# Kernel optimization log

Hardware: AMD Instinct MI355X
Metric: run time of the kernel (lower is better)

Reference implementation:

```python
import jax, jax.numpy as jnp
import numpy as np
import math

B, LQ, LK = 8, 1024, 1024
D_MODEL, NHEAD = 512, 8
DH = D_MODEL // NHEAD
FACTOR = 5
U = FACTOR * int(np.ceil(np.log(LQ)))  # 35: Informer's sample_k == n_top here (L_Q == L_K)


def _ln(x, g, b, eps=1e-5):
    m = x.mean(-1, keepdims=True)
    v = ((x - m) ** 2).mean(-1, keepdims=True)
    return (x - m) / jnp.sqrt(v + eps) * g + b


def _heads(x):  # (B,L,D) -> (B,H,L,Dh)
    Bx, L, _ = x.shape
    return x.reshape(Bx, L, NHEAD, DH).transpose(0, 2, 1, 3)


def _merge(x):  # (B,H,L,Dh) -> (B,L,D)
    Bx, H, L, Dh = x.shape
    return x.transpose(0, 2, 1, 3).reshape(Bx, L, H * Dh)


def _prob_attn(q, k, v, index_sample):
    # Informer ProbAttention, mask_flag=False. q,k,v: (B,H,L,Dh)
    Bx, H, Lq, Dh = q.shape
    Lk = k.shape[2]
    k_samp = k[:, :, index_sample, :]                        # (B,H,Lq,U,Dh) gathered keys
    qk_samp = jnp.einsum('bhld,bhlud->bhlu', q, k_samp)      # sampled scores
    M = qk_samp.max(-1) - qk_samp.sum(-1) / Lk               # sparsity measurement (B,H,Lq)
    _, top = jax.lax.top_k(M, U)                             # (B,H,U) top-u query indices
    q_red = jnp.take_along_axis(q, top[..., None], axis=2)   # (B,H,U,Dh)
    scores = jnp.einsum('bhud,bhkd->bhuk', q_red, k) * (1.0 / math.sqrt(Dh))
    attn = jax.nn.softmax(scores, axis=-1)
    upd = jnp.einsum('bhuk,bhkd->bhud', attn, v)             # (B,H,U,Dh)
    # initial context = mean of V (non-causal branch), then scatter top-u rows
    ctx = jnp.broadcast_to(v.mean(2, keepdims=True), (Bx, H, Lq, Dh))
    bi = jnp.arange(Bx)[:, None, None]
    hi = jnp.arange(H)[None, :, None]
    ctx = ctx.at[bi, hi, top].set(upd)
    return ctx


def _full_attn(q, k, v):
    s = jnp.einsum('bhld,bhsd->bhls', q, k) * (1.0 / math.sqrt(q.shape[-1]))
    a = jax.nn.softmax(s, axis=-1)
    return jnp.einsum('bhls,bhsd->bhld', a, v)


def setup_inputs():
    key = jax.random.key(0)
    ks = jax.random.split(key, 40)
    d = {}
    d['tgt'] = jax.random.normal(ks[0], (B, LQ, D_MODEL), jnp.float32)
    d['memory'] = jax.random.normal(ks[1], (B, LK, D_MODEL), jnp.float32)
    d['index_sample'] = jax.random.randint(ks[2], (LQ, U), 0, LK)
    i = 3
    for pre in ('1', '2'):
        for n in ('q', 'k', 'v', 'o'):
            d['w%s%s' % (n, pre)] = jax.random.normal(ks[i], (D_MODEL, D_MODEL), jnp.float32) * 0.02
            d['b%s%s' % (n, pre)] = jnp.zeros((D_MODEL,), jnp.float32)
            i += 1
    d['conv1_w'] = jax.random.normal(ks[i], (D_MODEL, 4 * D_MODEL), jnp.float32) * 0.02; i += 1
    d['conv1_b'] = jnp.zeros((4 * D_MODEL,), jnp.float32)
    d['conv2_w'] = jax.random.normal(ks[i], (4 * D_MODEL, D_MODEL), jnp.float32) * 0.02; i += 1
    d['conv2_b'] = jnp.zeros((D_MODEL,), jnp.float32)
    for n in ('ln1', 'ln2', 'ln3'):
        d[n + '_g'] = jnp.ones((D_MODEL,), jnp.float32)
        d[n + '_b'] = jnp.zeros((D_MODEL,), jnp.float32)
    return d


def reference(tgt, memory, index_sample, wq1, bq1, wk1, bk1, wv1, bv1, wo1, bo1,
              wq2, bq2, wk2, bk2, wv2, bv2, wo2, bo2,
              conv1_w, conv1_b, conv2_w, conv2_b,
              ln1_g, ln1_b, ln2_g, ln2_b, ln3_g, ln3_b):
    # dropout layers are identity (eval mode)
    x = tgt
    q = _heads(x @ wq1 + bq1)
    k = _heads(x @ wk1 + bk1)
    v = _heads(x @ wv1 + bv1)
    xn = _merge(_prob_attn(q, k, v, index_sample)) @ wo1 + bo1   # ProbSparse self-attn
    x = _ln(x + xn, ln1_g, ln1_b)                                # norm_enc1, with residual
    q = _heads(x @ wq2 + bq2)
    k = _heads(memory @ wk2 + bk2)
    v = _heads(memory @ wv2 + bv2)
    x = _merge(_full_attn(q, k, v)) @ wo2 + bo2                  # full cross-attn (no residual, per source)
    y = x = _ln(x, ln2_g, ln2_b)                                 # norm_enc2
    y = jax.nn.relu(y @ conv1_w + conv1_b) @ conv2_w + conv2_b   # conv1x1 FFN
    return _ln(x + y, ln3_g, ln3_b)                              # norm_enc3
```

## Files before the change

kernel.cpp:

```cpp
#include <hip/hip_runtime.h>
#include <hip/hip_bf16.h>
#include <cstdint>

constexpr int Bb  = 8;
constexpr int Ls  = 1024;
constexpr int DM  = 512;
constexpr int NH  = 8;
constexpr int DHd = 64;
constexpr int MR  = Bb * Ls;
constexpr int ZH  = Bb * NH;

typedef __attribute__((ext_vector_type(8))) short short8v;
typedef __attribute__((ext_vector_type(4))) short short4v;
typedef __attribute__((ext_vector_type(4))) float floatx4;

__device__ inline short f2bf(float x) {
  __hip_bfloat16 h = __float2bfloat16(x);
  return *reinterpret_cast<short*>(&h);
}
__device__ inline float bf2f(short s) {
  return __uint_as_float(((uint32_t)(uint16_t)s) << 16);
}

#define GLOAD_LDS16(g, l)                                                        \
  __builtin_amdgcn_global_load_lds(                                              \
      (const __attribute__((address_space(1))) void*)(g),                        \
      (__attribute__((address_space(3))) void*)(l), 16, 0, 0)

template<int MODE, int RELU>
__global__ __launch_bounds__(256) void k_gemm_mfma(
    const __hip_bfloat16* __restrict__ A, const __hip_bfloat16* __restrict__ Wt,
    const float* __restrict__ bias, const float* __restrict__ bias1,
    const float* __restrict__ bias2,
    void* __restrict__ Cout, void* __restrict__ aux1, void* __restrict__ aux2,
    void* __restrict__ aux3,
    int M, int N, int K)
{
  __shared__ __hip_bfloat16 As[2][128 * 32];
  __shared__ __hip_bfloat16 Bs[2][128 * 32];
  const int tid = threadIdx.x;
  const int w = tid >> 6, lane = tid & 63;
  const int wr = w >> 1, wc = w & 1;
  const int bm = blockIdx.x * 128, bn = blockIdx.y * 128;
  const int lrow = lane >> 2;
  const int lcol = (lane & 3) * 8;
  const int fr = lane & 15;
  const int fco = (lane >> 4) * 8;

  const __hip_bfloat16* Asrc = A;
  if (MODE == 12 && bn >= 512) Asrc = (const __hip_bfloat16*)aux3;

  const int ksl = K / gridDim.z;
  const int kb0 = blockIdx.z * ksl;
  const int nst = ksl / 32;

  const int chunk0 = w * 2, chunk1 = w * 2 + 1;
  const size_t aoff0 = (size_t)(bm + chunk0 * 16 + lrow) * K + lcol;
  const size_t aoff1 = (size_t)(bm + chunk1 * 16 + lrow) * K + lcol;
  const size_t boff0 = (size_t)(bn + chunk0 * 16 + lrow) * K + lcol;
  const size_t boff1 = (size_t)(bn + chunk1 * 16 + lrow) * K + lcol;

  {
    const int k0 = kb0;
    GLOAD_LDS16(Asrc + aoff0 + k0, &As[0][chunk0 * 512]);
    GLOAD_LDS16(Asrc + aoff1 + k0, &As[0][chunk1 * 512]);
    GLOAD_LDS16(Wt + boff0 + k0, &Bs[0][chunk0 * 512]);
    GLOAD_LDS16(Wt + boff1 + k0, &Bs[0][chunk1 * 512]);
  }
  asm volatile("s_waitcnt vmcnt(0)" ::: "memory");
  __builtin_amdgcn_s_barrier();

  floatx4 acc[4][4] = {};
  int cur = 0;
  for (int t = 0; t < nst; ++t) {
    if (t + 1 < nst) {
      const int k0 = kb0 + (t + 1) * 32;
      GLOAD_LDS16(Asrc + aoff0 + k0, &As[cur ^ 1][chunk0 * 512]);
      GLOAD_LDS16(Asrc + aoff1 + k0, &As[cur ^ 1][chunk1 * 512]);
      GLOAD_LDS16(Wt + boff0 + k0, &Bs[cur ^ 1][chunk0 * 512]);
      GLOAD_LDS16(Wt + boff1 + k0, &Bs[cur ^ 1][chunk1 * 512]);
    }
    const short* Ash = (const short*)As[cur];
    const short* Bsh = (const short*)Bs[cur];
    short8v a[4], b[4];
#pragma unroll
    for (int mi = 0; mi < 4; ++mi)
      a[mi] = *(const short8v*)(Ash + (wr * 64 + mi * 16 + fr) * 32 + fco);
#pragma unroll
    for (int ni = 0; ni < 4; ++ni)
      b[ni] = *(const short8v*)(Bsh + (wc * 64 + ni * 16 + fr) * 32 + fco);
#pragma unroll
    for (int mi = 0; mi < 4; ++mi)
#pragma unroll
      for (int ni = 0; ni < 4; ++ni)
        acc[mi][ni] = __builtin_amdgcn_mfma_f32_16x16x32_bf16(
            a[mi], b[ni], acc[mi][ni], 0, 0, 0);
    asm volatile("s_waitcnt vmcnt(0)" ::: "memory");
    __builtin_amdgcn_s_barrier();
    cur ^= 1;
  }
#pragma unroll
  for (int ni = 0; ni < 4; ++ni) {
    const int cn = bn + wc * 64 + ni * 16 + fr;
    float bv = 0.f;
    if (MODE == 10 || MODE == 12) {
      const float* bp = (cn < 512) ? bias : (cn < 1024 ? bias1 : bias2);
      bv = bp[cn & 511];
    } else if (MODE != 20) {
      bv = bias[cn];
    }
#pragma unroll
    for (int mi = 0; mi < 4; ++mi) {
      const int rm0 = bm + wr * 64 + mi * 16 + (lane >> 4) * 4;
      float vv[4];
#pragma unroll
      for (int j = 0; j < 4; ++j) {
        float v = acc[mi][ni][j] + bv;
        if (RELU) v = fmaxf(v, 0.f);
        vv[j] = v;
      }
      if (MODE == 1) {
#pragma unroll
        for (int j = 0; j < 4; ++j)
          ((__hip_bfloat16*)Cout)[(size_t)(rm0 + j) * N + cn] = __float2bfloat16(vv[j]);
      } else if (MODE == 10) {
        const int sel = cn >> 9, c = cn & 511;
        if (sel == 2) {
#pragma unroll
          for (int j = 0; j < 4; ++j)
            ((float*)aux2)[(size_t)(rm0 + j) * 512 + c] = vv[j];
        } else {
          const int hh = c >> 6, dd = c & 63;
          const int bb = rm0 >> 10, l0 = rm0 & 1023;
          __hip_bfloat16* bb16 = (__hip_bfloat16*)aux3 +
                                 (sel ? (size_t)ZH * Ls * 64 : 0);
#pragma unroll
          for (int j = 0; j < 4; ++j)
            bb16[(((size_t)(bb * 8 + hh)) * 1024 + l0 + j) * 64 + dd] =
                __float2bfloat16(vv[j]);
        }
      } else if (MODE == 12) {
        const int sel = cn >> 9, c = cn & 511;
        if (sel == 0) {
#pragma unroll
          for (int j = 0; j < 4; ++j)
            ((__hip_bfloat16*)Cout)[(size_t)(rm0 + j) * 512 + c] =
                __float2bfloat16(vv[j] * 0.125f);
        } else if (sel == 1) {
          const int cs = (c & ~63) | ((c & 63) ^ ((rm0 & 7) << 3));
#pragma unroll
          for (int j = 0; j < 4; ++j) {
            const int rm = rm0 + j;
            const int cj = (c & ~63) | ((c & 63) ^ ((rm & 7) << 3));
            ((__hip_bfloat16*)aux1)[(size_t)rm * 512 + cj] = __float2bfloat16(vv[j]);
          }
          (void)cs;
        } else {
          const int hh = c >> 6, dd = c & 63;
          const int bb = rm0 >> 10, l0 = rm0 & 1023;
          short4v pk;
#pragma unroll
          for (int j = 0; j < 4; ++j) pk[j] = f2bf(vv[j]);
          *(short4v*)((__hip_bfloat16*)aux2 +
                      (size_t)((bb * 8 + hh) * 64 + dd) * 1024 +
                      ((l0 ^ ((dd & 7) << 3)))) = pk;
        }
      } else if (MODE == 20) {
        float* pz = (float*)(blockIdx.z == 0 ? Cout :
                    blockIdx.z == 1 ? aux1 :
                    blockIdx.z == 2 ? aux2 : aux3);
#pragma unroll
        for (int j = 0; j < 4; ++j)
          pz[(size_t)(rm0 + j) * N + cn] = vv[j];
      }
    }
  }
}

__global__ __launch_bounds__(512) void k_flash2(
    const __hip_bfloat16* __restrict__ Qb,
    const __hip_bfloat16* __restrict__ Kb,
    const __hip_bfloat16* __restrict__ Vt,
    __hip_bfloat16* __restrict__ O)
{
  __shared__ __hip_bfloat16 Ks[2][64 * 64];
  __shared__ __hip_bfloat16 Vs[2][64 * 64];
  __shared__ __hip_bfloat16 Ps[8 * 16 * 72];
  const int tid = threadIdx.x, w = tid >> 6, lane = tid & 63;
  const int g = lane >> 4, r = lane & 15;
  const int z = blockIdx.y, b = z >> 3, h = z & 7;
  const int q0 = blockIdx.x * 128 + w * 16;
  __hip_bfloat16* Pw = Ps + w * 16 * 72;

  const int srow = w * 8 + (lane >> 3);
  const int sseg = lane & 7;

  const short8v qf0 = *(const short8v*)(Qb + (size_t)(b * Ls + q0 + r) * DM + h * DHd + g * 8);
  const short8v qf1 = *(const short8v*)(Qb + (size_t)(b * Ls + q0 + r) * DM + h * DHd + 32 + g * 8);

  floatx4 oacc[4] = {};
  float m_run = -1e30f, l_run = 0.f;

  GLOAD_LDS16(Kb + (size_t)(b * Ls + srow) * DM + h * DHd + sseg * 8, &Ks[0][w * 512]);
  GLOAD_LDS16(Vt + ((size_t)z * DHd + srow) * Ls + sseg * 8, &Vs[0][w * 512]);
  asm volatile("s_waitcnt vmcnt(0)" ::: "memory");
  __builtin_amdgcn_s_barrier();

  int cur = 0;
  for (int t = 0; t < 16; ++t) {
    if (t + 1 < 16) {
      GLOAD_LDS16(Kb + (size_t)(b * Ls + (t + 1) * 64 + srow) * DM + h * DHd + sseg * 8,
                  &Ks[cur ^ 1][w * 512]);
      GLOAD_LDS16(Vt + ((size_t)z * DHd + srow) * Ls + (t + 1) * 64 + sseg * 8,
                  &Vs[cur ^ 1][w * 512]);
    }
    const __hip_bfloat16* Kc = Ks[cur];
    const __hip_bfloat16* Vc = Vs[cur];
    float sv[4][4];
    float tmax = -1e30f;
    __builtin_amdgcn_s_setprio(1);
#pragma unroll
    for (int kt = 0; kt < 4; ++kt) {
      const int key = kt * 16 + r, sw = key & 7;
      short8v a0 = *(const short8v*)(Kc + key * 64 + ((g ^ sw) * 8));
      short8v a1 = *(const short8v*)(Kc + key * 64 + (((4 + g) ^ sw) * 8));
      floatx4 c = {};
      c = __builtin_amdgcn_mfma_f32_16x16x32_bf16(a0, qf0, c, 0, 0, 0);
      c = __builtin_amdgcn_mfma_f32_16x16x32_bf16(a1, qf1, c, 0, 0, 0);
#pragma unroll
      for (int j = 0; j < 4; ++j) {
        float x = c[j];
        sv[kt][j] = x;
        tmax = fmaxf(tmax, x);
      }
    }
    __builtin_amdgcn_s_setprio(0);
    tmax = fmaxf(tmax, __shfl_xor(tmax, 16));
    tmax = fmaxf(tmax, __shfl_xor(tmax, 32));
    float m_new;
    if (__all(tmax <= m_run + 8.0f)) {
      m_new = m_run;
    } else {
      m_new = fmaxf(m_run, tmax);
      const float fac = __expf(m_run - m_new);
      float fj[4];
#pragma unroll
      for (int j = 0; j < 4; ++j) fj[j] = __shfl(fac, (lane & 48) | (g * 4 + j));
#pragma unroll
      for (int ct = 0; ct < 4; ++ct)
#pragma unroll
        for (int j = 0; j < 4; ++j) oacc[ct][j] *= fj[j];
      l_run *= fac;
    }
    float psum = 0.f;
#pragma unroll
    for (int kt = 0; kt < 4; ++kt) {
      short4v pk;
#pragma unroll
      for (int j = 0; j < 4; ++j) {
        float p = __expf(sv[kt][j] - m_new);
        psum += p;
        pk[j] = f2bf(p);
      }
      *(short4v*)(Pw + r * 72 + kt * 16 + g * 4) = pk;
    }
    psum += __shfl_xor(psum, 16);
    psum += __shfl_xor(psum, 32);
    l_run += psum;
    m_run = m_new;
    const short8v pa0 = *(const short8v*)(Pw + r * 72 + g * 8);
    const short8v pa1 = *(const short8v*)(Pw + r * 72 + 32 + g * 8);
    __builtin_amdgcn_s_setprio(1);
#pragma unroll
    for (int ct = 0; ct < 4; ++ct) {
      const int d = ct * 16 + r, sw = d & 7;
      short8v v0 = *(const short8v*)(Vc + d * 64 + ((g ^ sw) * 8));
      short8v v1 = *(const short8v*)(Vc + d * 64 + (((4 + g) ^ sw) * 8));
      oacc[ct] = __builtin_amdgcn_mfma_f32_16x16x32_bf16(pa0, v0, oacc[ct], 0, 0, 0);
      oacc[ct] = __builtin_amdgcn_mfma_f32_16x16x32_bf16(pa1, v1, oacc[ct], 0, 0, 0);
    }
    __builtin_amdgcn_s_setprio(0);
    asm volatile("s_waitcnt vmcnt(0)" ::: "memory");
    __builtin_amdgcn_s_barrier();
    cur ^= 1;
  }
  float li[4];
#pragma unroll
  for (int j = 0; j < 4; ++j)
    li[j] = 1.0f / __shfl(l_run, (lane & 48) | (g * 4 + j));
#pragma unroll
  for (int ct = 0; ct < 4; ++ct)
#pragma unroll
    for (int j = 0; j < 4; ++j)
      O[(size_t)(b * Ls + q0 + g * 4 + j) * DM + h * DHd + ct * 16 + r] =
          __float2bfloat16(oacc[ct][j] * li[j]);
}

struct CvtArgs { const float* s[12]; __hip_bfloat16* d[12]; };
__global__ __launch_bounds__(256) void k_cvt_all(CvtArgs a)
{
  const int bid = blockIdx.x, tid = threadIdx.x;
  if (bid < 8192) {
    const size_t half = (size_t)MR * DM / 4;
    size_t i = (size_t)bid * 256 + tid;
    const float* in = a.s[10]; __hip_bfloat16* out = a.d[10];
    if (i >= half) { i -= half; in = a.s[11]; out = a.d[11]; }
    float4 v = *reinterpret_cast<const float4*>(in + i * 4);
    short4v o;
    o.x = f2bf(v.x); o.y = f2bf(v.y); o.z = f2bf(v.z); o.w = f2bf(v.w);
    *reinterpret_cast<short4v*>(out + i * 4) = o;
    return;
  }
  __shared__ float t[32][33];
  const int wb = bid - 8192;
  int widx, K, N, kblk, nblk;
  if (wb < 2048) {
    widx = wb >> 8; const int w2 = wb & 255;
    K = 512; N = 512; kblk = w2 & 15; nblk = w2 >> 4;
  } else if (wb < 3072) {
    widx = 8; const int w2 = wb - 2048;
    K = 512; N = 2048; kblk = w2 & 15; nblk = w2 >> 4;
  } else {
    widx = 9; const int w2 = wb - 3072;
    K = 2048; N = 512; kblk = w2 & 63; nblk = w2 >> 6;
  }
  const float* W = a.s[widx];
  __hip_bfloat16* Wt = a.d[widx];
  const int k0 = kblk * 32, n0 = nblk * 32;
  const int r = tid >> 3, c = (tid & 7) * 4;
  float4 v = *reinterpret_cast<const float4*>(W + (size_t)(k0 + r) * N + n0 + c);
  t[r][c + 0] = v.x; t[r][c + 1] = v.y; t[r][c + 2] = v.z; t[r][c + 3] = v.w;
  __syncthreads();
  short4v o;
  o.x = f2bf(t[c + 0][r]); o.y = f2bf(t[c + 1][r]);
  o.z = f2bf(t[c + 2][r]); o.w = f2bf(t[c + 3][r]);
  *reinterpret_cast<short4v*>(Wt + (size_t)(n0 + r) * K + k0 + c) = o;
}

__global__ __launch_bounds__(256) void k_probflash(
    const __hip_bfloat16* __restrict__ Qzb, const __hip_bfloat16* __restrict__ Kzb,
    const float* __restrict__ Vm, const int* __restrict__ top,
    float* __restrict__ Op, float* __restrict__ Ml, float* __restrict__ Ll,
    float* __restrict__ mvp, int U)
{
  __shared__ float Qs[DHd][64 + 4];
  __shared__ float Ks[DHd][64 + 4];
  __shared__ float Vs[64][64];
  __shared__ float ps[4][64];
  const int bid = blockIdx.x;
  const int swz = (bid & 7) * ((16 * ZH) >> 3) + (bid >> 3);
  const int kc = swz & 15, z = swz >> 4, b = z >> 3, h = z & 7;
  const int tid = threadIdx.x;
  const int k0 = kc * 64;
#pragma unroll
  for (int i = 0; i < 4; ++i) {
    const int idx = tid + (i << 8);
    const int r = idx >> 4, c4 = (idx & 15) << 2;
    int u = r; if (u >= U) u = U - 1;
    const int qr = top[z * U + u];
    short4v q4 = *reinterpret_cast<const short4v*>(Qzb + ((size_t)z * Ls + qr) * 64 + c4);
    Qs[c4 + 0][r] = bf2f(q4.x); Qs[c4 + 1][r] = bf2f(q4.y);
    Qs[c4 + 2][r] = bf2f(q4.z); Qs[c4 + 3][r] = bf2f(q4.w);
    short4v k4 = *reinterpret_cast<const short4v*>(Kzb + ((size_t)z * Ls + k0 + r) * 64 + c4);
    Ks[c4 + 0][r] = bf2f(k4.x); Ks[c4 + 1][r] = bf2f(k4.y);
    Ks[c4 + 2][r] = bf2f(k4.z); Ks[c4 + 3][r] = bf2f(k4.w);
    *reinterpret_cast<float4*>(&Vs[r][c4]) =
        *reinterpret_cast<const float4*>(Vm + ((size_t)(b * Ls + k0 + r)) * DM + h * DHd + c4);
  }
  __syncthreads();
  const int mB = (tid >> 4) << 2, nB = (tid & 15) << 2;
  float acc[4][4] = {};
#pragma unroll
  for (int kk = 0; kk < DHd; ++kk) {
    float4 a4 = *reinterpret_cast<const float4*>(&Qs[kk][mB]);
    float4 b4 = *reinterpret_cast<const float4*>(&Ks[kk][nB]);
    const float av[4] = {a4.x, a4.y, a4.z, a4.w};
#pragma unroll
    for (int i = 0; i < 4; ++i) {
      acc[i][0] += av[i] * b4.x; acc[i][1] += av[i] * b4.y;
      acc[i][2] += av[i] * b4.z; acc[i][3] += av[i] * b4.w;
    }
  }
  __syncthreads();
  float (*Ss)[68] = (float (*)[68])Qs;
#pragma unroll
  for (int i = 0; i < 4; ++i) {
    float4 o;
    o.x = acc[i][0] * 0.125f; o.y = acc[i][1] * 0.125f;
    o.z = acc[i][2] * 0.125f; o.w = acc[i][3] * 0.125f;
    *reinterpret_cast<float4*>(&Ss[mB + i][nB]) = o;
  }
  __syncthreads();
  {
    const int row = tid >> 2, q = tid & 3;
    float mx = -1e30f;
#pragma unroll
    for (int j = 0; j < 16; ++j) mx = fmaxf(mx, Ss[row][q * 16 + j]);
    mx = fmaxf(mx, __shfl_xor(mx, 1));
    mx = fmaxf(mx, __shfl_xor(mx, 2));
    float se = 0.f;
#pragma unroll
    for (int j = 0; j < 16; ++j) {
      float p = __expf(Ss[row][q * 16 + j] - mx);
      Ss[row][q * 16 + j] = p;
      se += p;
    }
    se += __shfl_xor(se, 1);
    se += __shfl_xor(se, 2);
    if (q == 0) {
      Ml[((size_t)kc * ZH + z) * 64 + row] = mx;
      Ll[((size_t)kc * ZH + z) * 64 + row] = se;
    }
  }
  __syncthreads();
  const int d = tid & 63, w = tid >> 6;
  {
    float s = 0.f;
#pragma unroll
    for (int i = 0; i < 16; ++i) s += Vs[w * 16 + i][d];
    ps[w][d] = s;
  }
  float acc2[16] = {};
  for (int k = 0; k < 64; ++k) {
    const float vk = Vs[k][d];
#pragma unroll
    for (int i = 0; i < 16; ++i)
      acc2[i] += Ss[w * 16 + i][k] * vk;
  }
  float* outb = Op + ((size_t)kc * ZH + z) * 4096;
#pragma unroll
  for (int i = 0; i < 16; ++i)
    outb[(w * 16 + i) * 64 + d] = acc2[i];
  __syncthreads();
  if (w == 0)
    mvp[((size_t)z * 16 + kc) * 64 + d] = ps[0][d] + ps[1][d] + ps[2][d] + ps[3][d];
}

__global__ __launch_bounds__(256) void k_prob_comb2(
    const float* __restrict__ Op, const float* __restrict__ Ml,
    const float* __restrict__ Ll, const int* __restrict__ top,
    const float* __restrict__ mvp, __hip_bfloat16* __restrict__ ctx, int U)
{
  __shared__ float wsh[16][64];
  __shared__ float Lsh[64];
  __shared__ short4v mvb[16];
  const int z = blockIdx.x, b = z >> 3, h = z & 7;
  const int tid = threadIdx.x;
  if (tid < 64) {
    float M = -1e30f;
#pragma unroll
    for (int c = 0; c < 16; ++c)
      M = fmaxf(M, Ml[((size_t)c * ZH + z) * 64 + tid]);
    float L = 0.f;
#pragma unroll
    for (int c = 0; c < 16; ++c) {
      float wv = __expf(Ml[((size_t)c * ZH + z) * 64 + tid] - M);
      wsh[c][tid] = wv;
      L += wv * Ll[((size_t)c * ZH + z) * 64 + tid];
    }
    Lsh[tid] = L;
    float s = 0.f;
#pragma unroll
    for (int c = 0; c < 16; ++c) s += mvp[((size_t)z * 16 + c) * 64 + tid];
    const short mb = f2bf(s * (1.0f / Ls));
    ((short*)mvb)[tid] = mb;
  }
  __syncthreads();
  __hip_bfloat16* base = ctx + (size_t)(b * Ls) * DM + h * DHd;
  for (int i = tid; i < 1024 * 16; i += 256) {
    const int row = i >> 4, c4 = i & 15;
    *reinterpret_cast<short4v*>(base + (size_t)row * DM + c4 * 4) = mvb[c4];
  }
  __syncthreads();
  for (int e = tid; e < U * 64; e += 256) {
    const int u = e >> 6, d = e & 63;
    float s = 0.f;
#pragma unroll
    for (int c = 0; c < 16; ++c)
      s += wsh[c][u] * Op[((size_t)c * ZH + z) * 4096 + u * 64 + d];
    const int row = top[z * U + u];
    ctx[((size_t)(b * Ls + row)) * DM + h * DHd + d] =
        __float2bfloat16(s / Lsh[u]);
  }
}

template<int UU>
__global__ __launch_bounds__(256) void k_mscore4(
    const __hip_bfloat16* __restrict__ Qzb, const __hip_bfloat16* __restrict__ Kzb,
    const int* __restrict__ smp, float* __restrict__ Ms)
{
  const int bid = blockIdx.x;
  const int swz = (bid & 7) * 256 + (bid >> 3);
  const int gw = swz * 4 + (threadIdx.x >> 6);
  const int lane = threadIdx.x & 63;
  const int li = lane >> 3, dp = (lane & 7) * 8;
  const int l = (gw & 127) * 8 + li;
  const int z = gw >> 7;
  const short8v q8 = *(const short8v*)(Qzb + ((size_t)z * Ls + l) * 64 + dp);
  float qf[8];
#pragma unroll
  for (int j = 0; j < 8; ++j) qf[j] = bf2f(q8[j]);
  int kidx[UU];
#pragma unroll
  for (int u = 0; u < UU; ++u) kidx[u] = smp[l * UU + u];
  const __hip_bfloat16* kzb = Kzb + (size_t)z * Ls * 64 + dp;
  float mx = -1e30f, sm = 0.f;
#pragma unroll
  for (int u = 0; u < UU; ++u) {
    const short8v k8 = *(const short8v*)(kzb + (size_t)kidx[u] * 64);
    float d = qf[0] * bf2f(k8[0]) + qf[1] * bf2f(k8[1])
            + qf[2] * bf2f(k8[2]) + qf[3] * bf2f(k8[3])
            + qf[4] * bf2f(k8[4]) + qf[5] * bf2f(k8[5])
            + qf[6] * bf2f(k8[6]) + qf[7] * bf2f(k8[7]);
    d += __shfl_xor(d, 1);
    d += __shfl_xor(d, 2);
    d += __shfl_xor(d, 4);
    mx = fmaxf(mx, d);
    sm += d;
  }
  if ((lane & 7) == 0) Ms[z * Ls + l] = mx - sm * (1.0f / Ls);
}

__global__ __launch_bounds__(256) void k_mscore4g(
    const __hip_bfloat16* __restrict__ Qzb, const __hip_bfloat16* __restrict__ Kzb,
    const int* __restrict__ smp, float* __restrict__ Ms, int U)
{
  const int bid = blockIdx.x;
  const int swz = (bid & 7) * 256 + (bid >> 3);
  const int gw = swz * 4 + (threadIdx.x >> 6);
  const int lane = threadIdx.x & 63;
  const int li = lane >> 3, dp = (lane & 7) * 8;
  const int l = (gw & 127) * 8 + li;
  const int z = gw >> 7;
  const short8v q8 = *(const short8v*)(Qzb + ((size_t)z * Ls + l) * 64 + dp);
  float qf[8];
#pragma unroll
  for (int j = 0; j < 8; ++j) qf[j] = bf2f(q8[j]);
  const __hip_bfloat16* kzb = Kzb + (size_t)z * Ls * 64 + dp;
  float mx = -1e30f, sm = 0.f;
  for (int u = 0; u < U; ++u) {
    const short8v k8 = *(const short8v*)(kzb + (size_t)smp[l * U + u] * 64);
    float d = qf[0] * bf2f(k8[0]) + qf[1] * bf2f(k8[1])
            + qf[2] * bf2f(k8[2]) + qf[3] * bf2f(k8[3])
            + qf[4] * bf2f(k8[4]) + qf[5] * bf2f(k8[5])
            + qf[6] * bf2f(k8[6]) + qf[7] * bf2f(k8[7]);
    d += __shfl_xor(d, 1);
    d += __shfl_xor(d, 2);
    d += __shfl_xor(d, 4);
    mx = fmaxf(mx, d);
    sm += d;
  }
  if ((lane & 7) == 0) Ms[z * Ls + l] = mx - sm * (1.0f / Ls);
}

__global__ __launch_bounds__(64) void k_topk_w(
    const float* __restrict__ Ms, int* __restrict__ top, int U)
{
  const int z = blockIdx.x, lane = threadIdx.x;
  float v[16];
#pragma unroll
  for (int j = 0; j < 16; ++j) v[j] = Ms[z * Ls + j * 64 + lane];
  for (int it = 0; it < U; ++it) {
    float bv = -1e30f; int bi = 0x7fffffff;
#pragma unroll
    for (int j = 0; j < 16; ++j) {
      const int idx = j * 64 + lane;
      if (v[j] > bv) { bv = v[j]; bi = idx; }
    }
#pragma unroll
    for (int off = 1; off < 64; off <<= 1) {
      const float ov = __shfl_xor(bv, off);
      const int   oi = __shfl_xor(bi, off);
      if (ov > bv || (ov == bv && oi < bi)) { bv = ov; bi = oi; }
    }
    if (lane == 0) top[z * U + it] = bi;
    if ((bi & 63) == lane) v[bi >> 6] = -1e30f;
  }
}

template<int NP>
__global__ __launch_bounds__(256) void k_ln2(
    const float* __restrict__ x0, const float* __restrict__ x1,
    const float* __restrict__ x2, const float* __restrict__ x3,
    const float* __restrict__ res, const float* __restrict__ bias,
    const float* __restrict__ g, const float* __restrict__ be,
    float* __restrict__ outf, __hip_bfloat16* __restrict__ outb)
{
  __shared__ float red[4];
  const int row = blockIdx.x, tid = threadIdx.x;
  const size_t base = (size_t)row * DM;
  float2 v = *reinterpret_cast<const float2*>(x0 + base + tid * 2);
  if (NP > 1) {
    float2 a = *reinterpret_cast<const float2*>(x1 + base + tid * 2);
    v.x += a.x; v.y += a.y;
  }
  if (NP > 2) {
    float2 a = *reinterpret_cast<const float2*>(x2 + base + tid * 2);
    v.x += a.x; v.y += a.y;
  }
  if (NP > 3) {
    float2 a = *reinterpret_cast<const float2*>(x3 + base + tid * 2);
    v.x += a.x; v.y += a.y;
  }
  if (bias) {
    float2 a = *reinterpret_cast<const float2*>(bias + tid * 2);
    v.x += a.x; v.y += a.y;
  }
  if (res) {
    float2 r2 = *reinterpret_cast<const float2*>(res + base + tid * 2);
    v.x += r2.x; v.y += r2.y;
  }
  float s = v.x + v.y;
#pragma unroll
  for (int off = 32; off; off >>= 1) s += __shfl_xor(s, off);
  if ((tid & 63) == 0) red[tid >> 6] = s;
  __syncthreads();
  s = red[0] + red[1] + red[2] + red[3];
  const float mean = s * (1.0f / DM);
  __syncthreads();
  float dx = v.x - mean, dy = v.y - mean;
  float q = dx * dx + dy * dy;
#pragma unroll
  for (int off = 32; off; off >>= 1) q += __shfl_xor(q, off);
  if ((tid & 63) == 0) red[tid >> 6] = q;
  __syncthreads();
  q = red[0] + red[1] + red[2] + red[3];
  const float inv = rsqrtf(q * (1.0f / DM) + 1e-5f);
  float2 gg = *reinterpret_cast<const float2*>(g + tid * 2);
  float2 bb = *reinterpret_cast<const float2*>(be + tid * 2);
  float ox = dx * inv * gg.x + bb.x;
  float oy = dy * inv * gg.y + bb.y;
  if (outf) {
    float2 o; o.x = ox; o.y = oy;
    *reinterpret_cast<float2*>(outf + base + tid * 2) = o;
  }
  if (outb) {
    short2 ob; ob.x = f2bf(ox); ob.y = f2bf(oy);
    *reinterpret_cast<short2*>(outb + base + tid * 2) = ob;
  }
}

extern "C" void kernel_launch(void* const* d_in, const int* in_sizes, int n_in,
                              void* d_out, int out_size, void* d_ws, size_t ws_size,
                              hipStream_t stream)
{
  const float* tgt = (const float*)d_in[0];
  const float* mem = (const float*)d_in[1];
  const int*   smp = (const int*)d_in[2];
  const float* wq1 = (const float*)d_in[3];  const float* bq1 = (const float*)d_in[4];
  const float* wk1 = (const float*)d_in[5];  const float* bk1 = (const float*)d_in[6];
  const float* wv1 = (const float*)d_in[7];  const float* bv1 = (const float*)d_in[8];
  const float* wo1 = (const float*)d_in[9];  const float* bo1 = (const float*)d_in[10];
  const float* wq2 = (const float*)d_in[11]; const float* bq2 = (const float*)d_in[12];
  const float* wk2 = (const float*)d_in[13]; const float* bk2 = (const float*)d_in[14];
  const float* wv2 = (const float*)d_in[15]; const float* bv2 = (const float*)d_in[16];
  const float* wo2 = (const float*)d_in[17]; const float* bo2 = (const float*)d_in[18];
  const float* c1w = (const float*)d_in[19]; const float* c1b = (const float*)d_in[20];
  const float* c2w = (const float*)d_in[21]; const float* c2b = (const float*)d_in[22];
  const float* g1  = (const float*)d_in[23]; const float* be1 = (const float*)d_in[24];
  const float* g2  = (const float*)d_in[25]; const float* be2 = (const float*)d_in[26];
  const float* g3  = (const float*)d_in[27]; const float* be3 = (const float*)d_in[28];
  float* outp = (float*)d_out;

  const int U   = in_sizes[2] / Ls;

  char* ws = (char*)d_ws;
  const size_t SZ = (size_t)MR * DM * sizeof(float);
  float* W0   = (float*)(ws);
  float* W1   = (float*)(ws + SZ);
  float* W2   = (float*)(ws + 2 * SZ);
  float* Sbuf = (float*)(ws + 3 * SZ);
  float* Op   = Sbuf + (size_t)ZH * 64 * Ls;
  __hip_bfloat16* QKzb = (__hip_bfloat16*)Sbuf;
  __hip_bfloat16* Qzb = QKzb;
  __hip_bfloat16* Kzb = QKzb + (size_t)ZH * Ls * 64;
  __hip_bfloat16* Tb  = (__hip_bfloat16*)(ws + 5 * SZ);
  __hip_bfloat16* Mb  = (__hip_bfloat16*)(ws + 5 * SZ + SZ / 2);
  __hip_bfloat16* Xb  = (__hip_bfloat16*)(ws + 6 * SZ);
  __hip_bfloat16* Vtb = (__hip_bfloat16*)(ws + 6 * SZ + SZ / 2);
  __hip_bfloat16* Wt3 = Vtb;
  char* tail = ws + 7 * SZ;
  __hip_bfloat16* wo1b = (__hip_bfloat16*)tail; tail += DM * DM * 2;
  __hip_bfloat16* wq2b = (__hip_bfloat16*)tail; tail += DM * DM * 2;
  __hip_bfloat16* wk2b = (__hip_bfloat16*)tail; tail += DM * DM * 2;
  __hip_bfloat16* wv2b = (__hip_bfloat16*)tail; tail += DM * DM * 2;
  __hip_bfloat16* wo2b = (__hip_bfloat16*)tail; tail += DM * DM * 2;
  __hip_bfloat16* c1wb = (__hip_bfloat16*)tail; tail += DM * 4 * DM * 2;
  __hip_bfloat16* c2wb = (__hip_bfloat16*)tail; tail += DM * 4 * DM * 2;
  float* Ms  = (float*)tail; tail += (size_t)ZH * Ls * 4;
  int*   top = (int*)tail;   tail += (size_t)ZH * 64 * 4;
  float* mvp = (float*)tail; tail += (size_t)ZH * 16 * DHd * 4;
  float* Ml  = (float*)tail; tail += (size_t)16 * ZH * 64 * 4;
  float* Ll  = (float*)tail; tail += (size_t)16 * ZH * 64 * 4;
  __hip_bfloat16* Kb = Tb;
  __hip_bfloat16* Qb = (__hip_bfloat16*)d_out;
  __hip_bfloat16* hb = (__hip_bfloat16*)Sbuf;

  CvtArgs ca;
  ca.s[0] = wq1; ca.d[0] = Wt3;
  ca.s[1] = wk1; ca.d[1] = Wt3 + DM * DM;
  ca.s[2] = wv1; ca.d[2] = Wt3 + 2 * DM * DM;
  ca.s[3] = wo1; ca.d[3] = wo1b;
  ca.s[4] = wq2; ca.d[4] = wq2b;
  ca.s[5] = wk2; ca.d[5] = wk2b;
  ca.s[6] = wv2; ca.d[6] = wv2b;
  ca.s[7] = wo2; ca.d[7] = wo2b;
  ca.s[8] = c1w; ca.d[8] = c1wb;
  ca.s[9] = c2w; ca.d[9] = c2wb;
  ca.s[10] = tgt; ca.d[10] = Tb;
  ca.s[11] = mem; ca.d[11] = Mb;
  k_cvt_all<<<dim3(12288), 256, 0, stream>>>(ca);

  k_gemm_mfma<10, 0><<<dim3(MR / 128, 12), 256, 0, stream>>>(
      Tb, Wt3, bq1, bk1, bv1, nullptr, nullptr, W2, QKzb, MR, 1536, DM);

  if (U == 35)
    k_mscore4<35><<<dim3(2048), 256, 0, stream>>>(Qzb, Kzb, smp, Ms);
  else
    k_mscore4g<<<dim3(2048), 256, 0, stream>>>(Qzb, Kzb, smp, Ms, U);
  k_topk_w<<<dim3(ZH), 64, 0, stream>>>(Ms, top, U);
  k_probflash<<<dim3(16 * ZH), 256, 0, stream>>>(Qzb, Kzb, W2, top, Op, Ml, Ll, mvp, U);
  k_prob_comb2<<<dim3(ZH), 256, 0, stream>>>(Op, Ml, Ll, top, mvp, Xb, U);

  k_gemm_mfma<20, 0><<<dim3(MR / 128, DM / 128, 2), 256, 0, stream>>>(
      Xb, wo1b, nullptr, nullptr, nullptr, W0, W1, nullptr, nullptr, MR, DM, DM);
  k_ln2<2><<<dim3(MR), 256, 0, stream>>>(W0, W1, nullptr, nullptr,
                                         tgt, bo1, g1, be1, nullptr, Xb);

  k_gemm_mfma<12, 0><<<dim3(MR / 128, 12), 256, 0, stream>>>(
      Xb, wq2b, bq2, bk2, bv2, Qb, Kb, Vtb, (void*)Mb, MR, 1536, DM);

  k_flash2<<<dim3(Ls / 128, ZH), 512, 0, stream>>>(Qb, Kb, Vtb, Xb);

  k_gemm_mfma<20, 0><<<dim3(MR / 128, DM / 128, 2), 256, 0, stream>>>(
      Xb, wo2b, nullptr, nullptr, nullptr, W0, W2, nullptr, nullptr, MR, DM, DM);
  k_ln2<2><<<dim3(MR), 256, 0, stream>>>(W0, W2, nullptr, nullptr,
                                         nullptr, bo2, g2, be2, W1, Xb);

  k_gemm_mfma<1, 1><<<dim3(MR / 128, 4 * DM / 128), 256, 0, stream>>>(
      Xb, c1wb, c1b, nullptr, nullptr, hb, nullptr, nullptr, nullptr, MR, 4 * DM, DM);
  k_gemm_mfma<20, 0><<<dim3(MR / 128, DM / 128, 2), 256, 0, stream>>>(
      hb, c2wb, nullptr, nullptr, nullptr, W0, W2, nullptr, nullptr, MR, DM, 2 * DM * 2);
  k_ln2<2><<<dim3(MR), 256, 0, stream>>>(W0, W2, nullptr, nullptr,
                                         W1, c2b, g3, be3, outp, nullptr);
}
```

Measured before the change: 304.4 us.

## Triple-buffer GEMM LDS staging with two-deep prefetch and MFMA priority boost

The MFMA GEMM moves from double to triple buffered LDS tiles. Loads are issued two k-steps ahead, and partial vmcnt waits let the next tile's loads stay in flight across the barrier. MFMA sections are wrapped in s_setprio to favour compute issue. This uses more LDS per block, which can lower occupancy. The MODE 20 split-K output now picks from only two buffers, which assumes gridDim.z is at most 2.

```diff
diff --git a/kernel.cpp b/kernel.cpp
--- a/kernel.cpp
+++ b/kernel.cpp
@@ -36,8 +36,8 @@
     void* __restrict__ aux3,
     int M, int N, int K)
 {
-  __shared__ __hip_bfloat16 As[2][128 * 32];
-  __shared__ __hip_bfloat16 Bs[2][128 * 32];
+  __shared__ __hip_bfloat16 As[3][128 * 32];
+  __shared__ __hip_bfloat16 Bs[3][128 * 32];
   const int tid = threadIdx.x;
   const int w = tid >> 6, lane = tid & 63;
   const int wr = w >> 1, wc = w & 1;
@@ -60,28 +60,30 @@
   const size_t boff0 = (size_t)(bn + chunk0 * 16 + lrow) * K + lcol;
   const size_t boff1 = (size_t)(bn + chunk1 * 16 + lrow) * K + lcol;
 
-  {
-    const int k0 = kb0;
-    GLOAD_LDS16(Asrc + aoff0 + k0, &As[0][chunk0 * 512]);
-    GLOAD_LDS16(Asrc + aoff1 + k0, &As[0][chunk1 * 512]);
-    GLOAD_LDS16(Wt + boff0 + k0, &Bs[0][chunk0 * 512]);
-    GLOAD_LDS16(Wt + boff1 + k0, &Bs[0][chunk1 * 512]);
-  }
-  asm volatile("s_waitcnt vmcnt(0)" ::: "memory");
+#define STAGE(tt, bf)                                                     \
+  {                                                                       \
+    const int k0s = kb0 + (tt) * 32;                                      \
+    GLOAD_LDS16(Asrc + aoff0 + k0s, &As[bf][chunk0 * 512]);               \
+    GLOAD_LDS16(Asrc + aoff1 + k0s, &As[bf][chunk1 * 512]);               \
+    GLOAD_LDS16(Wt + boff0 + k0s, &Bs[bf][chunk0 * 512]);                 \
+    GLOAD_LDS16(Wt + boff1 + k0s, &Bs[bf][chunk1 * 512]);                 \
+  }
+
+  STAGE(0, 0);
+  if (nst > 1) {
+    STAGE(1, 1);
+    asm volatile("s_waitcnt vmcnt(4)" ::: "memory");
+  } else {
+    asm volatile("s_waitcnt vmcnt(0)" ::: "memory");
+  }
   __builtin_amdgcn_s_barrier();
 
   floatx4 acc[4][4] = {};
-  int cur = 0;
+  int cb = 0, ib = 2;
   for (int t = 0; t < nst; ++t) {
-    if (t + 1 < nst) {
-      const int k0 = kb0 + (t + 1) * 32;
-      GLOAD_LDS16(Asrc + aoff0 + k0, &As[cur ^ 1][chunk0 * 512]);
-      GLOAD_LDS16(Asrc + aoff1 + k0, &As[cur ^ 1][chunk1 * 512]);
-      GLOAD_LDS16(Wt + boff0 + k0, &Bs[cur ^ 1][chunk0 * 512]);
-      GLOAD_LDS16(Wt + boff1 + k0, &Bs[cur ^ 1][chunk1 * 512]);
-    }
-    const short* Ash = (const short*)As[cur];
-    const short* Bsh = (const short*)Bs[cur];
+    if (t + 2 < nst) STAGE(t + 2, ib);
+    const short* Ash = (const short*)As[cb];
+    const short* Bsh = (const short*)Bs[cb];
     short8v a[4], b[4];
 #pragma unroll
     for (int mi = 0; mi < 4; ++mi)
@@ -89,16 +91,25 @@
 #pragma unroll
     for (int ni = 0; ni < 4; ++ni)
       b[ni] = *(const short8v*)(Bsh + (wc * 64 + ni * 16 + fr) * 32 + fco);
+    __builtin_amdgcn_s_setprio(1);
 #pragma unroll
     for (int mi = 0; mi < 4; ++mi)
 #pragma unroll
       for (int ni = 0; ni < 4; ++ni)
         acc[mi][ni] = __builtin_amdgcn_mfma_f32_16x16x32_bf16(
             a[mi], b[ni], acc[mi][ni], 0, 0, 0);
-    asm volatile("s_waitcnt vmcnt(0)" ::: "memory");
-    __builtin_amdgcn_s_barrier();
-    cur ^= 1;
-  }
+    __builtin_amdgcn_s_setprio(0);
+    if (t + 1 < nst) {
+      if (t + 2 < nst)
+        asm volatile("s_waitcnt vmcnt(4)" ::: "memory");
+      else
+        asm volatile("s_waitcnt vmcnt(0)" ::: "memory");
+      __builtin_amdgcn_s_barrier();
+    }
+    cb = (cb == 2) ? 0 : cb + 1;
+    ib = (ib == 2) ? 0 : ib + 1;
+  }
+#undef STAGE
 #pragma unroll
   for (int ni = 0; ni < 4; ++ni) {
     const int cn = bn + wc * 64 + ni * 16 + fr;
@@ -147,14 +158,12 @@
             ((__hip_bfloat16*)Cout)[(size_t)(rm0 + j) * 512 + c] =
                 __float2bfloat16(vv[j] * 0.125f);
         } else if (sel == 1) {
-          const int cs = (c & ~63) | ((c & 63) ^ ((rm0 & 7) << 3));
 #pragma unroll
           for (int j = 0; j < 4; ++j) {
             const int rm = rm0 + j;
             const int cj = (c & ~63) | ((c & 63) ^ ((rm & 7) << 3));
             ((__hip_bfloat16*)aux1)[(size_t)rm * 512 + cj] = __float2bfloat16(vv[j]);
           }
-          (void)cs;
         } else {
           const int hh = c >> 6, dd = c & 63;
           const int bb = rm0 >> 10, l0 = rm0 & 1023;
@@ -166,9 +175,7 @@
                       ((l0 ^ ((dd & 7) << 3)))) = pk;
         }
       } else if (MODE == 20) {
-        float* pz = (float*)(blockIdx.z == 0 ? Cout :
-                    blockIdx.z == 1 ? aux1 :
-                    blockIdx.z == 2 ? aux2 : aux3);
+        float* pz = (float*)(blockIdx.z == 0 ? Cout : aux1);
 #pragma unroll
         for (int j = 0; j < 4; ++j)
           pz[(size_t)(rm0 + j) * N + cn] = vv[j];
```

New measurement: 309.9 us. No clear change (+1.8%).
